# Performance work log

Hardware: AMD Instinct MI355X
Metric: run time of the kernel (lower is better)

## Reference

```python
import jax, jax.numpy as jnp
import numpy as np

DIM = 256
HEADS = 8
HD = DIM // HEADS  # 32
WS = 8             # window size
N = WS * WS        # 64 tokens per window
BN_SCALE = 1.0 / np.sqrt(1.0 + 1e-5)  # BatchNorm with default running stats (mean 0, var 1)


def _relative_position_index():
    # static int index table [N, N], computed with numpy (matches torch buffer)
    coords = np.stack(np.meshgrid(np.arange(WS), np.arange(WS), indexing='ij'))  # (2, ws, ws)
    cf = coords.reshape(2, -1)                                                   # (2, N)
    rel = cf[:, :, None] - cf[:, None, :]                                        # (2, N, N)
    rel = rel.transpose(1, 2, 0)                                                 # (N, N, 2)
    rel[:, :, 0] += WS - 1
    rel[:, :, 1] += WS - 1
    rel[:, :, 0] *= 2 * WS - 1
    return jnp.asarray(rel.sum(-1))  # (N, N)


def _relative_coords_table():
    # static float table [(2ws-1), (2ws-1), 2] with Swin-V2 log-spaced coords
    r = np.arange(-(WS - 1), WS, dtype=np.float32)
    g = np.stack(np.meshgrid(r, r, indexing='ij'), axis=-1)  # (L, L, 2)
    g = g / (WS - 1) * 8.0
    g = np.sign(g) * np.log2(np.abs(g) + 1.0) / np.log2(8.0)
    return jnp.asarray(g)


def setup_inputs() -> dict:
    key = jax.random.key(0)
    ks = jax.random.split(key, 9)
    B, H, W = 16, 64, 64
    s = 0.02
    return {
        'x': jax.random.normal(ks[0], (B, DIM, H, W), dtype=jnp.float32),
        'qkv_w': jax.random.normal(ks[1], (3 * DIM, DIM), dtype=jnp.float32) * s,
        'qkv_b': jax.random.normal(ks[2], (3 * DIM,), dtype=jnp.float32) * s,
        'proj_w': jax.random.normal(ks[3], (DIM, DIM), dtype=jnp.float32) * s,
        'proj_b': jax.random.normal(ks[4], (DIM,), dtype=jnp.float32) * s,
        'cpb_w1': jax.random.normal(ks[5], (DIM, 2), dtype=jnp.float32) * 0.5,
        'cpb_b1': jax.random.normal(ks[6], (DIM,), dtype=jnp.float32) * 0.5,
        'cpb_w2': jax.random.normal(ks[7], (HEADS, DIM), dtype=jnp.float32) * 0.1,
        'dw_w': jax.random.normal(ks[8], (DIM, 1, 7, 7), dtype=jnp.float32) * s,
    }


def reference(x, qkv_w, qkv_b, proj_w, proj_b, cpb_w1, cpb_b1, cpb_w2, dw_w):
    B, C, H, W = x.shape
    Hn, Wn = H // WS, W // WS
    B_ = B * Hn * Wn

    # continuous position bias: pointwise MLP (conv1x1+BN+SiLU, conv1x1+BN)
    tbl = _relative_coords_table()                          # (L, L, 2)
    h = jax.nn.silu((tbl @ cpb_w1.T + cpb_b1) * BN_SCALE)   # (L, L, DIM)
    bias_table = (h @ cpb_w2.T) * BN_SCALE                  # (L, L, HEADS)
    bias_table = bias_table.reshape(-1, HEADS)
    rpi = _relative_position_index()
    bias = bias_table[rpi.reshape(-1)].reshape(N, N, HEADS).transpose(2, 0, 1)
    bias = 16.0 * jax.nn.sigmoid(bias)                      # (HEADS, N, N)

    # qkv 1x1 conv, window partition
    qkv = jnp.einsum('oc,bchw->bohw', qkv_w, x) + qkv_b[None, :, None, None]
    win = qkv.reshape(B, 3 * C, Hn, WS, Wn, WS).transpose(0, 2, 4, 1, 3, 5)
    win = win.reshape(B_, 3 * C, N)
    qkvw = win.reshape(B_, 3, HEADS, HD, N).transpose(1, 0, 2, 4, 3)  # (3, B_, H, N, hd)
    q, k, v = qkvw[0], qkvw[1], qkvw[2]

    # SDPA with additive bias (attn_mask)
    scores = jnp.einsum('bhnd,bhmd->bhnm', q, k) / np.sqrt(HD) + bias[None]
    attn = jax.nn.softmax(scores, axis=-1)
    o = jnp.einsum('bhnm,bhmd->bhnd', attn, v)

    def window_reverse(w):  # (B_, N, C) -> (B, C, H, W)
        t = w.reshape(B, Hn, Wn, WS, WS, C).transpose(0, 5, 1, 3, 2, 4)
        return t.reshape(B, C, H, W)

    x_img = window_reverse(o.transpose(0, 2, 1, 3).reshape(B_, N, C))
    v_img = window_reverse(v.transpose(0, 2, 1, 3).reshape(B_, N, C))

    # depthwise 7x7 positional encoding on v, residual add
    pe = jax.lax.conv_general_dilated(
        v_img, dw_w, window_strides=(1, 1), padding='SAME',
        feature_group_count=C, dimension_numbers=('NCHW', 'OIHW', 'NCHW'))
    out = x_img + pe
    out = jnp.einsum('oc,bchw->bohw', proj_w, out) + proj_b[None, :, None, None]
    return out
```

## Files before the change

kernel.cpp:

```cpp
#include <hip/hip_runtime.h>
#include <cstdint>
#include <cstddef>

typedef unsigned short u16;
typedef unsigned int   u32;

#define LW     15
#define BNS    0.9999950000374997f
#define SCALE  0.17677669529663687f

typedef __bf16 bf16x8 __attribute__((ext_vector_type(8)));
typedef float  f32x4  __attribute__((ext_vector_type(4)));
typedef u16    u16x8  __attribute__((ext_vector_type(8)));

__device__ __forceinline__ u16 f2bf(float f){
  union { float f; u32 i; } v; v.f = f;
  u32 r = v.i + 0x7FFFu + ((v.i >> 16) & 1u);
  return (u16)(r >> 16);
}
__device__ __forceinline__ float bf2f(u16 u){
  union { u32 i; float f; } v; v.i = ((u32)u) << 16; return v.f;
}

__global__ void k_cvt_w(const float* __restrict__ qw, const float* __restrict__ pw,
                        u16* __restrict__ qwb, u16* __restrict__ pwb){
  const int i = blockIdx.x*256 + threadIdx.x;
  if (i < 196608) qwb[i] = f2bf(qw[i]);
  else            pwb[i - 196608] = f2bf(pw[i - 196608]);
}

__global__ void k_cpb_mlp(const float* __restrict__ w1, const float* __restrict__ b1,
                          const float* __restrict__ w2, float* __restrict__ tab){
  const int e = blockIdx.x;
  const int c = threadIdx.x;
  const float a0 = (float)(e / LW - 7);
  const float a1 = (float)(e % LW - 7);
  const float cx = copysignf(log2f(fabsf(a0)*(8.f/7.f) + 1.f) * (1.f/3.f), a0);
  const float cy = copysignf(log2f(fabsf(a1)*(8.f/7.f) + 1.f) * (1.f/3.f), a1);
  float pre = (cx*w1[2*c] + cy*w1[2*c+1] + b1[c]) * BNS;
  float hid = pre / (1.f + __expf(-pre));
  __shared__ float hl[256];
  hl[c] = hid;
  __syncthreads();
  if (c < 8){
    float s = 0.f;
    for (int i = 0; i < 256; ++i) s += hl[i] * w2[c*256 + i];
    tab[e*8 + c] = s * BNS;
  }
}

__global__ void k_bias_expand(const float* __restrict__ tab, float* __restrict__ biasT){
  const int id = blockIdx.x*256 + threadIdx.x;
  const int nq = id & 63;
  const int m  = (id >> 6) & 63;
  const int h  = id >> 12;
  const int dy = (nq >> 3) - (m >> 3) + 7;
  const int dx = (nq & 7)  - (m & 7)  + 7;
  const float v = tab[(dy*LW + dx)*8 + h];
  biasT[id] = 16.f / (1.f + __expf(-v));
}

__global__ __launch_bounds__(256, 2) void k_qkv_attn(
    const float* __restrict__ x, const u16* __restrict__ qwb,
    const float* __restrict__ qb, const float* __restrict__ biasT,
    float* __restrict__ xout, u16* __restrict__ vout){
  const int win = blockIdx.x;
  const int b = win >> 6, wy = (win >> 3) & 7, wx = win & 7;
  __shared__ __align__(16) char smem[80384];
  u16*   xs   = (u16*)(smem);
  u16*   q_b  = (u16*)(smem + 33792);
  u16*   ks_  = (u16*)(smem + 52224);
  u16*   vsT  = (u16*)(smem + 70656);
  float* linv = (float*)(smem + 79872);

  const float* xbase = x + (size_t)b*256*4096 + (size_t)(wy*8)*64 + wx*8;
  for (int i = threadIdx.x; i < 4096; i += 256){
    const int c  = i >> 4;
    const int g  = i & 15;
    const int py = g >> 1, xh = (g & 1) * 4;
    float4 v4 = *(const float4*)&xbase[(size_t)c*4096 + py*64 + xh];
    const int n0 = py*8 + xh;
    xs[(n0+0)*264 + c] = f2bf(v4.x);
    xs[(n0+1)*264 + c] = f2bf(v4.y);
    xs[(n0+2)*264 + c] = f2bf(v4.z);
    xs[(n0+3)*264 + c] = f2bf(v4.w);
  }
  const int wave = threadIdx.x >> 6, lane = threadIdx.x & 63;
  const int quad = lane >> 4, l16 = lane & 15;

  const int ed = threadIdx.x >> 3;
  const int eq = (threadIdx.x & 7) * 8;
  const size_t epix = (size_t)(wy*8 + (threadIdx.x & 7))*64 + wx*8;

  const f32x4 zero4 = {0.f, 0.f, 0.f, 0.f};
  const int qn = wave*16 + l16;

  __syncthreads();

  for (int p = 0; p < 4; ++p){
    bf16x8 af[3][8];
    float4 bias4[3];
    #pragma unroll
    for (int j = 0; j < 3; ++j){
      const int rt  = wave*3 + j;
      const int sec = rt >> 2;
      const int hs  = (rt >> 1) & 1;
      const int dl  = (rt & 1) * 16;
      const int oga = sec*256 + (p*2 + hs)*32 + dl + l16;
      #pragma unroll
      for (int kc = 0; kc < 8; ++kc)
        af[j][kc] = *(const bf16x8*)(qwb + (size_t)oga*256 + kc*32 + quad*8);
      bias4[j] = *(const float4*)&qb[sec*256 + (p*2 + hs)*32 + dl + quad*4];
    }
    #pragma unroll
    for (int th = 0; th < 2; ++th){
      f32x4 acc[3][2];
      #pragma unroll
      for (int j = 0; j < 3; ++j){ acc[j][0] = zero4; acc[j][1] = zero4; }
      #pragma unroll
      for (int kc = 0; kc < 8; ++kc){
        bf16x8 b0 = *(const bf16x8*)&xs[((th*2+0)*16 + l16)*264 + kc*32 + quad*8];
        bf16x8 b1 = *(const bf16x8*)&xs[((th*2+1)*16 + l16)*264 + kc*32 + quad*8];
        #pragma unroll
        for (int j = 0; j < 3; ++j){
          acc[j][0] = __builtin_amdgcn_mfma_f32_16x16x32_bf16(af[j][kc], b0, acc[j][0], 0, 0, 0);
          acc[j][1] = __builtin_amdgcn_mfma_f32_16x16x32_bf16(af[j][kc], b1, acc[j][1], 0, 0, 0);
        }
      }
      #pragma unroll
      for (int j = 0; j < 3; ++j){
        const int rt  = wave*3 + j;
        const int sec = rt >> 2;
        const int hs  = (rt >> 1) & 1;
        const int dl  = (rt & 1) * 16;
        const int ddo = hs*32 + dl + quad*4;
        #pragma unroll
        for (int t2 = 0; t2 < 2; ++t2){
          const int tok = (th*2 + t2)*16 + l16;
          const f32x4 a = acc[j][t2];
          if (sec < 2){
            ushort4 pk;
            pk.x = f2bf(a[0] + bias4[j].x);
            pk.y = f2bf(a[1] + bias4[j].y);
            pk.z = f2bf(a[2] + bias4[j].z);
            pk.w = f2bf(a[3] + bias4[j].w);
            u16* dst = (sec == 0) ? q_b : ks_;
            *(ushort4*)&dst[tok*72 + ddo] = pk;
          } else {
            vsT[(ddo+0)*72 + tok] = f2bf(a[0] + bias4[j].x);
            vsT[(ddo+1)*72 + tok] = f2bf(a[1] + bias4[j].y);
            vsT[(ddo+2)*72 + tok] = f2bf(a[2] + bias4[j].z);
            vsT[(ddo+3)*72 + tok] = f2bf(a[3] + bias4[j].w);
          }
        }
      }
    }
    __syncthreads();

    bf16x8 qf2[2];
    qf2[0] = *(const bf16x8*)&q_b[qn*72 +  0 + quad*8];
    qf2[1] = *(const bf16x8*)&q_b[qn*72 + 32 + quad*8];
    #pragma unroll
    for (int h2 = 0; h2 < 2; ++h2){
      const int h = p*2 + h2;
      f32x4 st[4];
      #pragma unroll
      for (int kt = 0; kt < 4; ++kt){
        bf16x8 ka = *(const bf16x8*)&ks_[(kt*16 + l16)*72 + h2*32 + quad*8];
        st[kt] = __builtin_amdgcn_mfma_f32_16x16x32_bf16(ka, qf2[h2], zero4, 0, 0, 0);
      }
      float sc[16], mx = -1e30f;
      #pragma unroll
      for (int kt = 0; kt < 4; ++kt)
        #pragma unroll
        for (int r = 0; r < 4; ++r){
          const int key = kt*16 + quad*4 + r;
          const float v = st[kt][r]*SCALE + biasT[(h<<12) + (key<<6) + qn];
          sc[kt*4+r] = v; mx = fmaxf(mx, v);
        }
      mx = fmaxf(mx, __shfl_xor(mx, 16));
      mx = fmaxf(mx, __shfl_xor(mx, 32));
      float sum = 0.f;
      #pragma unroll
      for (int i = 0; i < 16; ++i){ sc[i] = __expf(sc[i] - mx); sum += sc[i]; }
      sum += __shfl_xor(sum, 16);
      sum += __shfl_xor(sum, 32);
      if (quad == 0) linv[h2*64 + qn] = 1.f / sum;
      u16* P = (u16*)(smem + 33792 + h2*9216);
      #pragma unroll
      for (int kt = 0; kt < 4; ++kt){
        ushort4 pk;
        pk.x = f2bf(sc[kt*4+0]); pk.y = f2bf(sc[kt*4+1]);
        pk.z = f2bf(sc[kt*4+2]); pk.w = f2bf(sc[kt*4+3]);
        *(ushort4*)&P[qn*72 + kt*16 + quad*4] = pk;
      }
    }
    __syncthreads();

    #pragma unroll
    for (int h2 = 0; h2 < 2; ++h2){
      const u16* P = (const u16*)(smem + 33792 + h2*9216);
      float* obuf  = (float*)(smem + 52224 + h2*9216);
      bf16x8 pa0 = *(const bf16x8*)&P[qn*72 +  0 + quad*8];
      bf16x8 pa1 = *(const bf16x8*)&P[qn*72 + 32 + quad*8];
      #pragma unroll
      for (int dt = 0; dt < 2; ++dt){
        bf16x8 bv0 = *(const bf16x8*)&vsT[(h2*32 + dt*16 + l16)*72 +  0 + quad*8];
        bf16x8 bv1 = *(const bf16x8*)&vsT[(h2*32 + dt*16 + l16)*72 + 32 + quad*8];
        f32x4 o = __builtin_amdgcn_mfma_f32_16x16x32_bf16(pa0, bv0, zero4, 0, 0, 0);
        o = __builtin_amdgcn_mfma_f32_16x16x32_bf16(pa1, bv1, o, 0, 0, 0);
        #pragma unroll
        for (int r = 0; r < 4; ++r){
          const float ls = linv[h2*64 + wave*16 + quad*4 + r];
          obuf[(dt*16 + l16)*72 + wave*16 + quad*4 + r] = o[r]*ls;
        }
      }
    }
    __syncthreads();

    #pragma unroll
    for (int h2 = 0; h2 < 2; ++h2){
      const float* obuf = (const float*)(smem + 52224 + h2*9216);
      const size_t gp = ((size_t)(b*256 + (p*2 + h2)*32 + ed))*4096 + epix;
      float4 o0 = *(const float4*)&obuf[ed*72 + eq];
      float4 o1 = *(const float4*)&obuf[ed*72 + eq + 4];
      *(float4*)&xout[gp]     = o0;
      *(float4*)&xout[gp + 4] = o1;
      u16x8 v8 = *(const u16x8*)&vsT[(h2*32 + ed)*72 + eq];
      *(u16x8*)&vout[gp] = v8;
    }
    __syncthreads();
  }
}

__global__ __launch_bounds__(256) void k_dwconv(
    const u16* __restrict__ vimg, const float* __restrict__ dww,
    float* __restrict__ io){
  const int b = blockIdx.x >> 8, c = blockIdx.x & 255;
  __shared__ float tile[70*72];
  const size_t base = ((size_t)(b*256 + c)) * 4096;
  for (int i = threadIdx.x; i < 1260; i += 256)
    *(float4*)&tile[i*4] = (float4){0.f, 0.f, 0.f, 0.f};
  float w[49];
  #pragma unroll
  for (int j = 0; j < 49; ++j) w[j] = dww[c*49 + j];
  __syncthreads();
  for (int i = threadIdx.x; i < 512; i += 256){
    const int y = i >> 3, x8 = (i & 7) * 8;
    u16x8 v = *(const u16x8*)&vimg[base + y*64 + x8];
    #pragma unroll
    for (int j = 0; j < 8; ++j) tile[(y+3)*72 + x8 + 3 + j] = bf2f(v[j]);
  }
  __syncthreads();

  const int x0 = (threadIdx.x & 15) * 4;
  const int y0 = (threadIdx.x >> 4) * 4;
  float acc[4][4];
  #pragma unroll
  for (int i = 0; i < 4; ++i)
    #pragma unroll
    for (int j = 0; j < 4; ++j) acc[i][j] = 0.f;

  #pragma unroll
  for (int ty = 0; ty < 10; ++ty){
    const float* rp = &tile[(y0 + ty)*72 + x0];
    float r[12];
    *(float4*)&r[0] = *(const float4*)&rp[0];
    *(float4*)&r[4] = *(const float4*)&rp[4];
    *(float4*)&r[8] = *(const float4*)&rp[8];
    #pragma unroll
    for (int oy = 0; oy < 4; ++oy){
      if (ty >= oy && ty - oy <= 6){
        const int ky = ty - oy;
        #pragma unroll
        for (int ox = 0; ox < 4; ++ox)
          #pragma unroll
          for (int kx = 0; kx < 7; ++kx)
            acc[oy][ox] += w[ky*7 + kx] * r[ox + kx];
      }
    }
  }
  #pragma unroll
  for (int oy = 0; oy < 4; ++oy){
    const size_t gi = base + (size_t)(y0 + oy)*64 + x0;
    float4 res = *(const float4*)&io[gi];
    res.x += acc[oy][0]; res.y += acc[oy][1];
    res.z += acc[oy][2]; res.w += acc[oy][3];
    *(float4*)&io[gi] = res;
  }
}

__global__ __launch_bounds__(256) void k_proj(
    const u16* __restrict__ pwb, const float* __restrict__ pb,
    float* __restrict__ io){
  const int row = blockIdx.x;
  const int b = row >> 6, y = row & 63;
  __shared__ __align__(16) u16 ts[64*264];
  const float* tbase = io + (size_t)b*256*4096 + (size_t)y*64;
  for (int i = threadIdx.x; i < 4096; i += 256){
    const int c = i >> 4, n0 = (i & 15) * 4;
    float4 v4 = *(const float4*)&tbase[(size_t)c*4096 + n0];
    ts[(n0+0)*264 + c] = f2bf(v4.x);
    ts[(n0+1)*264 + c] = f2bf(v4.y);
    ts[(n0+2)*264 + c] = f2bf(v4.z);
    ts[(n0+3)*264 + c] = f2bf(v4.w);
  }
  __syncthreads();
  const int wave = threadIdx.x >> 6, lane = threadIdx.x & 63;
  const int quad = lane >> 4, l16 = lane & 15;
  const f32x4 zero4 = {0.f, 0.f, 0.f, 0.f};
  #pragma unroll
  for (int op = 0; op < 2; ++op){
    bf16x8 af2[2][8];
    #pragma unroll
    for (int oj = 0; oj < 2; ++oj){
      const int orow = (wave*4 + op*2 + oj)*16 + l16;
      #pragma unroll
      for (int kc = 0; kc < 8; ++kc)
        af2[oj][kc] = *(const bf16x8*)(pwb + (size_t)orow*256 + kc*32 + quad*8);
    }
    f32x4 acc[2][4];
    #pragma unroll
    for (int oj = 0; oj < 2; ++oj)
      #pragma unroll
      for (int nt = 0; nt < 4; ++nt) acc[oj][nt] = zero4;
    #pragma unroll
    for (int kc = 0; kc < 8; ++kc){
      bf16x8 bf[4];
      #pragma unroll
      for (int nt = 0; nt < 4; ++nt)
        bf[nt] = *(const bf16x8*)&ts[(nt*16 + l16)*264 + kc*32 + quad*8];
      #pragma unroll
      for (int oj = 0; oj < 2; ++oj)
        #pragma unroll
        for (int nt = 0; nt < 4; ++nt)
          acc[oj][nt] = __builtin_amdgcn_mfma_f32_16x16x32_bf16(af2[oj][kc], bf[nt], acc[oj][nt], 0, 0, 0);
    }
    #pragma unroll
    for (int oj = 0; oj < 2; ++oj){
      const int ot = wave*4 + op*2 + oj;
      #pragma unroll
      for (int nt = 0; nt < 4; ++nt)
        #pragma unroll
        for (int r = 0; r < 4; ++r){
          const int o = ot*16 + quad*4 + r;
          io[((size_t)(b*256 + o))*4096 + (size_t)y*64 + nt*16 + l16] = acc[oj][nt][r] + pb[o];
        }
    }
  }
}

extern "C" void kernel_launch(void* const* d_in, const int* in_sizes, int n_in,
                              void* d_out, int out_size, void* d_ws, size_t ws_size,
                              hipStream_t stream){
  const float* x   = (const float*)d_in[0];
  const float* qw  = (const float*)d_in[1];
  const float* qb  = (const float*)d_in[2];
  const float* pw  = (const float*)d_in[3];
  const float* pb  = (const float*)d_in[4];
  const float* w1  = (const float*)d_in[5];
  const float* b1  = (const float*)d_in[6];
  const float* w2  = (const float*)d_in[7];
  const float* dww = (const float*)d_in[8];

  char* ws = (char*)d_ws;
  float* tab   = (float*)(ws);
  float* biasT = (float*)(ws + 8192);
  u16*   qwb   = (u16*)  (ws + 139264);
  u16*   pwb   = (u16*)  (ws + 532480);
  u16*   vimg  = (u16*)  (ws + 663552);
  float* out   = (float*)d_out;

  k_cvt_w      <<<1024, 256, 0, stream>>>(qw, pw, qwb, pwb);
  k_cpb_mlp    <<<225,  256, 0, stream>>>(w1, b1, w2, tab);
  k_bias_expand<<<128,  256, 0, stream>>>(tab, biasT);
  k_qkv_attn   <<<1024, 256, 0, stream>>>(x, qwb, qb, biasT, out, vimg);
  k_dwconv     <<<4096, 256, 0, stream>>>(vimg, dww, out);
  k_proj       <<<1024, 256, 0, stream>>>(pwb, pb, out);
}
```

Baseline: 321.3 us.

## Restructure window attention to one wave per head with 512-thread blocks

The fused QKV+attention kernel now runs 8 waves per block, each owning one head end-to-end. Each wave computes its own Q/K/V projection, softmax and PV product, and keeps intermediates in registers with a small per-wave LDS bounce buffer. This removes the four-pass head-pair loop and its many block-wide barriers. The bias table is re-laid out query-major for vectorized loads, the 1/sum normalization is folded into P before the PV MFMA, and outputs go straight to global memory. The cost is more register pressure from the launch bounds of (512,4), and the weight fragments for each head are loaded by its wave alone.

```diff
diff --git a/kernel.cpp b/kernel.cpp
--- a/kernel.cpp
+++ b/kernel.cpp
@@ -49,32 +49,32 @@
   }
 }
 
-__global__ void k_bias_expand(const float* __restrict__ tab, float* __restrict__ biasT){
+__global__ void k_bias_expand(const float* __restrict__ tab, float* __restrict__ biasQ){
   const int id = blockIdx.x*256 + threadIdx.x;
-  const int nq = id & 63;
-  const int m  = (id >> 6) & 63;
-  const int h  = id >> 12;
-  const int dy = (nq >> 3) - (m >> 3) + 7;
-  const int dx = (nq & 7)  - (m & 7)  + 7;
+  const int key = id & 63;
+  const int q   = (id >> 6) & 63;
+  const int h   = id >> 12;
+  const int dy = (q >> 3) - (key >> 3) + 7;
+  const int dx = (q & 7)  - (key & 7)  + 7;
   const float v = tab[(dy*LW + dx)*8 + h];
-  biasT[id] = 16.f / (1.f + __expf(-v));
-}
-
-__global__ __launch_bounds__(256, 2) void k_qkv_attn(
+  biasQ[id] = 16.f / (1.f + __expf(-v));
+}
+
+__global__ __launch_bounds__(512, 4) void k_qkv_attn(
     const float* __restrict__ x, const u16* __restrict__ qwb,
-    const float* __restrict__ qb, const float* __restrict__ biasT,
+    const float* __restrict__ qb, const float* __restrict__ biasQ,
     float* __restrict__ xout, u16* __restrict__ vout){
   const int win = blockIdx.x;
   const int b = win >> 6, wy = (win >> 3) & 7, wx = win & 7;
-  __shared__ __align__(16) char smem[80384];
-  u16*   xs   = (u16*)(smem);
-  u16*   q_b  = (u16*)(smem + 33792);
-  u16*   ks_  = (u16*)(smem + 52224);
-  u16*   vsT  = (u16*)(smem + 70656);
-  float* linv = (float*)(smem + 79872);
+  __shared__ __align__(16) char smem[70656];
+  u16* xs = (u16*)smem;
+  const int tid  = threadIdx.x;
+  const int wave = tid >> 6, lane = tid & 63;
+  const int quad = lane >> 4, l16 = lane & 15;
+  u16* vbw = (u16*)(smem + 33792 + wave*4608);
 
   const float* xbase = x + (size_t)b*256*4096 + (size_t)(wy*8)*64 + wx*8;
-  for (int i = threadIdx.x; i < 4096; i += 256){
+  for (int i = tid; i < 4096; i += 512){
     const int c  = i >> 4;
     const int g  = i & 15;
     const int py = g >> 1, xh = (g & 1) * 4;
@@ -85,151 +85,158 @@
     xs[(n0+2)*264 + c] = f2bf(v4.z);
     xs[(n0+3)*264 + c] = f2bf(v4.w);
   }
-  const int wave = threadIdx.x >> 6, lane = threadIdx.x & 63;
-  const int quad = lane >> 4, l16 = lane & 15;
-
-  const int ed = threadIdx.x >> 3;
-  const int eq = (threadIdx.x & 7) * 8;
-  const size_t epix = (size_t)(wy*8 + (threadIdx.x & 7))*64 + wx*8;
-
+  __syncthreads();
+
+  const int h = wave;
   const f32x4 zero4 = {0.f, 0.f, 0.f, 0.f};
-  const int qn = wave*16 + l16;
-
-  __syncthreads();
-
-  for (int p = 0; p < 4; ++p){
-    bf16x8 af[3][8];
-    float4 bias4[3];
-    #pragma unroll
-    for (int j = 0; j < 3; ++j){
-      const int rt  = wave*3 + j;
-      const int sec = rt >> 2;
-      const int hs  = (rt >> 1) & 1;
-      const int dl  = (rt & 1) * 16;
-      const int oga = sec*256 + (p*2 + hs)*32 + dl + l16;
-      #pragma unroll
-      for (int kc = 0; kc < 8; ++kc)
-        af[j][kc] = *(const bf16x8*)(qwb + (size_t)oga*256 + kc*32 + quad*8);
-      bias4[j] = *(const float4*)&qb[sec*256 + (p*2 + hs)*32 + dl + quad*4];
-    }
-    #pragma unroll
-    for (int th = 0; th < 2; ++th){
-      f32x4 acc[3][2];
-      #pragma unroll
-      for (int j = 0; j < 3; ++j){ acc[j][0] = zero4; acc[j][1] = zero4; }
-      #pragma unroll
-      for (int kc = 0; kc < 8; ++kc){
-        bf16x8 b0 = *(const bf16x8*)&xs[((th*2+0)*16 + l16)*264 + kc*32 + quad*8];
-        bf16x8 b1 = *(const bf16x8*)&xs[((th*2+1)*16 + l16)*264 + kc*32 + quad*8];
-        #pragma unroll
-        for (int j = 0; j < 3; ++j){
-          acc[j][0] = __builtin_amdgcn_mfma_f32_16x16x32_bf16(af[j][kc], b0, acc[j][0], 0, 0, 0);
-          acc[j][1] = __builtin_amdgcn_mfma_f32_16x16x32_bf16(af[j][kc], b1, acc[j][1], 0, 0, 0);
+
+  auto run_gemm = [&](int sec, u32 (&w)[2][4][2]){
+    f32x4 acc[2][4];
+    #pragma unroll
+    for (int rt = 0; rt < 2; ++rt)
+      #pragma unroll
+      for (int tt = 0; tt < 4; ++tt) acc[rt][tt] = zero4;
+    #pragma unroll
+    for (int kh2 = 0; kh2 < 2; ++kh2){
+      bf16x8 af[2][4];
+      #pragma unroll
+      for (int rt = 0; rt < 2; ++rt){
+        const int wr = sec*256 + h*32 + rt*16 + l16;
+        #pragma unroll
+        for (int kc = 0; kc < 4; ++kc)
+          af[rt][kc] = *(const bf16x8*)(qwb + (size_t)wr*256 + (kh2*4 + kc)*32 + quad*8);
+      }
+      #pragma unroll
+      for (int kc = 0; kc < 4; ++kc){
+        #pragma unroll
+        for (int tt = 0; tt < 4; ++tt){
+          bf16x8 bf = *(const bf16x8*)&xs[(tt*16 + l16)*264 + (kh2*4 + kc)*32 + quad*8];
+          acc[0][tt] = __builtin_amdgcn_mfma_f32_16x16x32_bf16(af[0][kc], bf, acc[0][tt], 0, 0, 0);
+          acc[1][tt] = __builtin_amdgcn_mfma_f32_16x16x32_bf16(af[1][kc], bf, acc[1][tt], 0, 0, 0);
         }
       }
-      #pragma unroll
-      for (int j = 0; j < 3; ++j){
-        const int rt  = wave*3 + j;
-        const int sec = rt >> 2;
-        const int hs  = (rt >> 1) & 1;
-        const int dl  = (rt & 1) * 16;
-        const int ddo = hs*32 + dl + quad*4;
-        #pragma unroll
-        for (int t2 = 0; t2 < 2; ++t2){
-          const int tok = (th*2 + t2)*16 + l16;
-          const f32x4 a = acc[j][t2];
-          if (sec < 2){
-            ushort4 pk;
-            pk.x = f2bf(a[0] + bias4[j].x);
-            pk.y = f2bf(a[1] + bias4[j].y);
-            pk.z = f2bf(a[2] + bias4[j].z);
-            pk.w = f2bf(a[3] + bias4[j].w);
-            u16* dst = (sec == 0) ? q_b : ks_;
-            *(ushort4*)&dst[tok*72 + ddo] = pk;
-          } else {
-            vsT[(ddo+0)*72 + tok] = f2bf(a[0] + bias4[j].x);
-            vsT[(ddo+1)*72 + tok] = f2bf(a[1] + bias4[j].y);
-            vsT[(ddo+2)*72 + tok] = f2bf(a[2] + bias4[j].z);
-            vsT[(ddo+3)*72 + tok] = f2bf(a[3] + bias4[j].w);
-          }
+    }
+    #pragma unroll
+    for (int rt = 0; rt < 2; ++rt){
+      float4 b4 = *(const float4*)&qb[sec*256 + h*32 + rt*16 + quad*4];
+      #pragma unroll
+      for (int tt = 0; tt < 4; ++tt){
+        w[rt][tt][0] = (u32)f2bf(acc[rt][tt][0] + b4.x) |
+                       ((u32)f2bf(acc[rt][tt][1] + b4.y) << 16);
+        w[rt][tt][1] = (u32)f2bf(acc[rt][tt][2] + b4.z) |
+                       ((u32)f2bf(acc[rt][tt][3] + b4.w) << 16);
+      }
+    }
+  };
+
+  auto bounce_td = [&](const u32 (&w)[2][4][2], bf16x8 (&frag)[4]){
+    #pragma unroll
+    for (int half = 0; half < 2; ++half){
+      #pragma unroll
+      for (int t2 = 0; t2 < 2; ++t2){
+        const int tt = half*2 + t2;
+        #pragma unroll
+        for (int rt = 0; rt < 2; ++rt)
+          #pragma unroll
+          for (int u = 0; u < 2; ++u)
+            *(u32*)&vbw[(t2*16 + l16)*40 + rt*16 + quad*4 + 2*u] = w[rt][tt][u];
+      }
+      #pragma unroll
+      for (int t2 = 0; t2 < 2; ++t2)
+        frag[half*2 + t2] = *(const bf16x8*)&vbw[(t2*16 + l16)*40 + quad*8];
+    }
+  };
+
+  bf16x8 qf[4], ka[4];
+  {
+    u32 wq[2][4][2];
+    run_gemm(0, wq);
+    bounce_td(wq, qf);
+  }
+  {
+    u32 wk[2][4][2];
+    run_gemm(1, wk);
+    bounce_td(wk, ka);
+  }
+
+  bf16x8 pa[4][2];
+  #pragma unroll
+  for (int qt = 0; qt < 4; ++qt){
+    f32x4 st[4];
+    #pragma unroll
+    for (int kt = 0; kt < 4; ++kt)
+      st[kt] = __builtin_amdgcn_mfma_f32_16x16x32_bf16(ka[kt], qf[qt], zero4, 0, 0, 0);
+    float4 bq[4];
+    #pragma unroll
+    for (int kt = 0; kt < 4; ++kt)
+      bq[kt] = *(const float4*)&biasQ[(h<<12) + (qt*16 + l16)*64 + kt*16 + quad*4];
+    float sc[16], mx = -1e30f;
+    #pragma unroll
+    for (int kt = 0; kt < 4; ++kt)
+      #pragma unroll
+      for (int r = 0; r < 4; ++r){
+        const float v = st[kt][r]*SCALE + ((const float*)&bq[kt])[r];
+        sc[kt*4+r] = v; mx = fmaxf(mx, v);
+      }
+    mx = fmaxf(mx, __shfl_xor(mx, 16));
+    mx = fmaxf(mx, __shfl_xor(mx, 32));
+    float sum = 0.f;
+    #pragma unroll
+    for (int i = 0; i < 16; ++i){ sc[i] = __expf(sc[i] - mx); sum += sc[i]; }
+    sum += __shfl_xor(sum, 16);
+    sum += __shfl_xor(sum, 32);
+    const float inv = 1.f / sum;
+    #pragma unroll
+    for (int kt = 0; kt < 4; ++kt){
+      u32 w0 = (u32)f2bf(sc[kt*4+0]*inv) | ((u32)f2bf(sc[kt*4+1]*inv) << 16);
+      u32 w1 = (u32)f2bf(sc[kt*4+2]*inv) | ((u32)f2bf(sc[kt*4+3]*inv) << 16);
+      *(u32*)&vbw[l16*72 + kt*16 + quad*4 + 0] = w0;
+      *(u32*)&vbw[l16*72 + kt*16 + quad*4 + 2] = w1;
+    }
+    pa[qt][0] = *(const bf16x8*)&vbw[l16*72 +  0 + quad*8];
+    pa[qt][1] = *(const bf16x8*)&vbw[l16*72 + 32 + quad*8];
+  }
+
+  {
+    u32 wv[2][4][2];
+    run_gemm(2, wv);
+    #pragma unroll
+    for (int rt = 0; rt < 2; ++rt)
+      #pragma unroll
+      for (int tt = 0; tt < 4; ++tt)
+        #pragma unroll
+        for (int u = 0; u < 2; ++u){
+          vbw[(rt*16 + quad*4 + 2*u + 0)*72 + tt*16 + l16] = (u16)(wv[rt][tt][u] & 0xFFFFu);
+          vbw[(rt*16 + quad*4 + 2*u + 1)*72 + tt*16 + l16] = (u16)(wv[rt][tt][u] >> 16);
         }
-      }
-    }
-    __syncthreads();
-
-    bf16x8 qf2[2];
-    qf2[0] = *(const bf16x8*)&q_b[qn*72 +  0 + quad*8];
-    qf2[1] = *(const bf16x8*)&q_b[qn*72 + 32 + quad*8];
-    #pragma unroll
-    for (int h2 = 0; h2 < 2; ++h2){
-      const int h = p*2 + h2;
-      f32x4 st[4];
-      #pragma unroll
-      for (int kt = 0; kt < 4; ++kt){
-        bf16x8 ka = *(const bf16x8*)&ks_[(kt*16 + l16)*72 + h2*32 + quad*8];
-        st[kt] = __builtin_amdgcn_mfma_f32_16x16x32_bf16(ka, qf2[h2], zero4, 0, 0, 0);
-      }
-      float sc[16], mx = -1e30f;
-      #pragma unroll
-      for (int kt = 0; kt < 4; ++kt)
-        #pragma unroll
-        for (int r = 0; r < 4; ++r){
-          const int key = kt*16 + quad*4 + r;
-          const float v = st[kt][r]*SCALE + biasT[(h<<12) + (key<<6) + qn];
-          sc[kt*4+r] = v; mx = fmaxf(mx, v);
-        }
-      mx = fmaxf(mx, __shfl_xor(mx, 16));
-      mx = fmaxf(mx, __shfl_xor(mx, 32));
-      float sum = 0.f;
-      #pragma unroll
-      for (int i = 0; i < 16; ++i){ sc[i] = __expf(sc[i] - mx); sum += sc[i]; }
-      sum += __shfl_xor(sum, 16);
-      sum += __shfl_xor(sum, 32);
-      if (quad == 0) linv[h2*64 + qn] = 1.f / sum;
-      u16* P = (u16*)(smem + 33792 + h2*9216);
-      #pragma unroll
-      for (int kt = 0; kt < 4; ++kt){
-        ushort4 pk;
-        pk.x = f2bf(sc[kt*4+0]); pk.y = f2bf(sc[kt*4+1]);
-        pk.z = f2bf(sc[kt*4+2]); pk.w = f2bf(sc[kt*4+3]);
-        *(ushort4*)&P[qn*72 + kt*16 + quad*4] = pk;
-      }
-    }
-    __syncthreads();
-
-    #pragma unroll
-    for (int h2 = 0; h2 < 2; ++h2){
-      const u16* P = (const u16*)(smem + 33792 + h2*9216);
-      float* obuf  = (float*)(smem + 52224 + h2*9216);
-      bf16x8 pa0 = *(const bf16x8*)&P[qn*72 +  0 + quad*8];
-      bf16x8 pa1 = *(const bf16x8*)&P[qn*72 + 32 + quad*8];
-      #pragma unroll
-      for (int dt = 0; dt < 2; ++dt){
-        bf16x8 bv0 = *(const bf16x8*)&vsT[(h2*32 + dt*16 + l16)*72 +  0 + quad*8];
-        bf16x8 bv1 = *(const bf16x8*)&vsT[(h2*32 + dt*16 + l16)*72 + 32 + quad*8];
-        f32x4 o = __builtin_amdgcn_mfma_f32_16x16x32_bf16(pa0, bv0, zero4, 0, 0, 0);
-        o = __builtin_amdgcn_mfma_f32_16x16x32_bf16(pa1, bv1, o, 0, 0, 0);
-        #pragma unroll
-        for (int r = 0; r < 4; ++r){
-          const float ls = linv[h2*64 + wave*16 + quad*4 + r];
-          obuf[(dt*16 + l16)*72 + wave*16 + quad*4 + r] = o[r]*ls;
-        }
-      }
-    }
-    __syncthreads();
-
-    #pragma unroll
-    for (int h2 = 0; h2 < 2; ++h2){
-      const float* obuf = (const float*)(smem + 52224 + h2*9216);
-      const size_t gp = ((size_t)(b*256 + (p*2 + h2)*32 + ed))*4096 + epix;
-      float4 o0 = *(const float4*)&obuf[ed*72 + eq];
-      float4 o1 = *(const float4*)&obuf[ed*72 + eq + 4];
-      *(float4*)&xout[gp]     = o0;
-      *(float4*)&xout[gp + 4] = o1;
-      u16x8 v8 = *(const u16x8*)&vsT[(h2*32 + ed)*72 + eq];
-      *(u16x8*)&vout[gp] = v8;
-    }
-    __syncthreads();
+  }
+  bf16x8 bv[2][2];
+  #pragma unroll
+  for (int dt = 0; dt < 2; ++dt)
+    #pragma unroll
+    for (int kh = 0; kh < 2; ++kh)
+      bv[dt][kh] = *(const bf16x8*)&vbw[(dt*16 + l16)*72 + kh*32 + quad*8];
+
+  {
+    const int d  = lane >> 1;
+    #pragma unroll
+    for (int i = 0; i < 4; ++i){
+      const int ch = (lane & 1)*4 + i;
+      u16x8 v8 = *(const u16x8*)&vbw[d*72 + ch*8];
+      *(u16x8*)&vout[((size_t)(b*256 + h*32 + d))*4096 + (size_t)(wy*8 + ch)*64 + wx*8] = v8;
+    }
+  }
+
+  #pragma unroll
+  for (int qt = 0; qt < 4; ++qt){
+    #pragma unroll
+    for (int dt = 0; dt < 2; ++dt){
+      f32x4 o = __builtin_amdgcn_mfma_f32_16x16x32_bf16(pa[qt][0], bv[dt][0], zero4, 0, 0, 0);
+      o = __builtin_amdgcn_mfma_f32_16x16x32_bf16(pa[qt][1], bv[dt][1], o, 0, 0, 0);
+      float4 o4; o4.x = o[0]; o4.y = o[1]; o4.z = o[2]; o4.w = o[3];
+      *(float4*)&xout[((size_t)(b*256 + h*32 + dt*16 + l16))*4096
+                      + (size_t)(wy*8 + qt*2 + (quad>>1))*64 + wx*8 + (quad&1)*4] = o4;
+    }
   }
 }
 
@@ -365,7 +372,7 @@
 
   char* ws = (char*)d_ws;
   float* tab   = (float*)(ws);
-  float* biasT = (float*)(ws + 8192);
+  float* biasQ = (float*)(ws + 8192);
   u16*   qwb   = (u16*)  (ws + 139264);
   u16*   pwb   = (u16*)  (ws + 532480);
   u16*   vimg  = (u16*)  (ws + 663552);
@@ -373,8 +380,8 @@
 
   k_cvt_w      <<<1024, 256, 0, stream>>>(qw, pw, qwb, pwb);
   k_cpb_mlp    <<<225,  256, 0, stream>>>(w1, b1, w2, tab);
-  k_bias_expand<<<128,  256, 0, stream>>>(tab, biasT);
-  k_qkv_attn   <<<1024, 256, 0, stream>>>(x, qwb, qb, biasT, out, vimg);
+  k_bias_expand<<<128,  256, 0, stream>>>(tab, biasQ);
+  k_qkv_attn   <<<1024, 512, 0, stream>>>(x, qwb, qb, biasQ, out, vimg);
   k_dwconv     <<<4096, 256, 0, stream>>>(vimg, dww, out);
   k_proj       <<<1024, 256, 0, stream>>>(pwb, pb, out);
 }
```

Measured after the change: 307.2 us. 1.05x faster.
